# Performance work log

Hardware: AMD Instinct MI355X
Metric: run time of the kernel (lower is better)

Reference implementation:

```python
import jax, jax.numpy as jnp
import numpy as np


def setup_inputs() -> dict:
    key = jax.random.key(0)
    N, D, K = 8192, 512, 16
    x = jax.random.normal(key, (N, D), dtype=jnp.float32)
    return {"x": x, "k": K}


def reference(x, k):
    # Pairwise Euclidean distances (torch.cdist(x, x)), computed via the
    # GEMM-based expansion ||a-b||^2 = ||a||^2 + ||b||^2 - 2 a.b
    sq = jnp.sum(x * x, axis=1)                      # [N]
    d2 = sq[:, None] + sq[None, :] - 2.0 * (x @ x.T)  # [N, N]
    dists = jnp.sqrt(jnp.maximum(d2, 0.0))

    # Nearest-neighbor indices per row (skip self at column 0, since
    # self-distance is exactly 0 and therefore sorts first).
    idxs = jnp.argsort(dists, axis=1)[:, 1:k + 1]    # [N, k]

    # Gather neighbor features and average: x_avg[i] = mean(x[idxs[i]], axis=0)
    x_avg = jnp.mean(x[idxs], axis=1)                # [N, D]
    return x_avg
```

## Files before the change

### kernel.cpp

```cpp
#include <hip/hip_runtime.h>
#include <hip/hip_bf16.h>

#define Nn 8192
#define Dd 512
#define KK 16
#define CC 24
#define CSUB 5
#define JSPLIT 32
#define PENT 256

typedef int i32x4 __attribute__((ext_vector_type(4)));
typedef unsigned int uint32;

__device__ __forceinline__ uint32 med3u(uint32 a, uint32 b, uint32 c) {
  uint32 d;
  asm("v_med3_u32 %0, %1, %2, %3" : "=v"(d) : "v"(a), "v"(b), "v"(c));
  return d;
}

template <int CCn>
__device__ __forceinline__ void topk_insert(uint32* h, uint32 v) {
#pragma unroll
  for (int s = 0; s < CCn - 1; ++s) h[s] = med3u(h[s], h[s + 1], v);
  h[CCn - 1] = (h[CCn - 1] < v) ? h[CCn - 1] : v;
}

__device__ __forceinline__ uint32 cswap(uint32 v, int j, bool asc, int lane) {
  uint32 pv = (uint32)__shfl_xor((int)v, j, 64);
  uint32 mn = v < pv ? v : pv;
  uint32 mx = v < pv ? pv : v;
  const bool lower = ((lane & j) == 0);
  return (asc == lower) ? mn : mx;
}

__device__ __forceinline__ void sort64(uint32& v, int lane) {
#pragma unroll
  for (int k = 2; k <= 32; k <<= 1) {
#pragma unroll
    for (int j = k >> 1; j > 0; j >>= 1) {
      const bool asc = ((lane & k) == 0);
      v = cswap(v, j, asc, lane);
    }
  }
#pragma unroll
  for (int j = 32; j > 0; j >>= 1) v = cswap(v, j, true, lane);
}

__device__ __forceinline__ void sort128(uint32& v0, uint32& v1, int lane) {
#pragma unroll
  for (int k = 2; k <= 32; k <<= 1) {
#pragma unroll
    for (int j = k >> 1; j > 0; j >>= 1) {
      const bool asc = ((lane & k) == 0);
      v0 = cswap(v0, j, asc, lane);
      v1 = cswap(v1, j, asc, lane);
    }
  }
#pragma unroll
  for (int j = 32; j > 0; j >>= 1) {
    v0 = cswap(v0, j, true, lane);
    v1 = cswap(v1, j, false, lane);
  }
  {
    uint32 mn = v0 < v1 ? v0 : v1;
    uint32 mx = v0 < v1 ? v1 : v0;
    v0 = mn;
    v1 = mx;
  }
#pragma unroll
  for (int j = 32; j > 0; j >>= 1) {
    v0 = cswap(v0, j, true, lane);
    v1 = cswap(v1, j, true, lane);
  }
}

__global__ void knn_prep(const float* __restrict__ x, uint4* __restrict__ xq,
                         float2* __restrict__ sqs) {
  __shared__ float redS[2][16][17];
  const int rb = blockIdx.x;
  const int t = threadIdx.x;
  const int ccg = t & 15;
  const int r16 = t >> 4;
  const int row = rb * 16 + r16;
  float v[32];
  float s = 0.f, amax = 0.f;
#pragma unroll
  for (int h = 0; h < 2; ++h) {
    const int cc = h * 16 + ccg;
#pragma unroll
    for (int q = 0; q < 4; ++q) {
      float4 a = *(const float4*)&x[(size_t)row * Dd + cc * 16 + q * 4];
      v[h * 16 + q * 4 + 0] = a.x;
      v[h * 16 + q * 4 + 1] = a.y;
      v[h * 16 + q * 4 + 2] = a.z;
      v[h * 16 + q * 4 + 3] = a.w;
      s = fmaf(a.x, a.x, s); s = fmaf(a.y, a.y, s);
      s = fmaf(a.z, a.z, s); s = fmaf(a.w, a.w, s);
      amax = fmaxf(amax, fmaxf(fmaxf(fabsf(a.x), fabsf(a.y)),
                               fmaxf(fabsf(a.z), fabsf(a.w))));
    }
  }
  redS[0][r16][ccg] = s;
  redS[1][r16][ccg] = amax;
  __syncthreads();
  float tot = 0.f, mx = 0.f;
#pragma unroll
  for (int i = 0; i < 16; ++i) {
    tot += redS[0][r16][i];
    mx = fmaxf(mx, redS[1][r16][i]);
  }
  const float inv = (mx > 0.f) ? (127.f / mx) : 0.f;
  if (ccg == 0) sqs[row] = make_float2(tot, mx * (1.f / 127.f));
#pragma unroll
  for (int h = 0; h < 2; ++h) {
    const int cc = h * 16 + ccg;
    uint32 wds[4];
#pragma unroll
    for (int q = 0; q < 4; ++q) {
      uint32 b = 0;
#pragma unroll
      for (int e = 0; e < 4; ++e) {
        int qi = __float2int_rn(v[h * 16 + q * 4 + e] * inv);
        b |= ((uint32)(qi & 0xFF)) << (8 * e);
      }
      wds[q] = b;
    }
    xq[((size_t)cc * 512 + rb) * 16 + r16] =
        make_uint4(wds[0], wds[1], wds[2], wds[3]);
  }
}

__global__ __launch_bounds__(256, 2) void knn_cand(
    const uint4* __restrict__ xqv, const float2* __restrict__ sqs,
    uint32* __restrict__ partials) {
  __shared__ uint32 entS[128][41];
  __shared__ uint32 hS[128][16];

  const int bid = blockIdx.x;
  const int xcd = bid & 7;
  const int jc = xcd * 4 + ((bid >> 3) & 3);
  const int ib = bid >> 5;
  const int t = threadIdx.x;
  const int w = t >> 6;
  const int l = t & 63;
  const int wrow = w >> 1, wcol = w & 1;
  const int l16 = l & 15, lq = l >> 4;

  const i32x4* xf = (const i32x4*)xqv;
  const int abase = ib * 8 + wrow * 4;
  const int bbase = jc * 16 + wcol * 8;
  const int jbase = jc * 256;

  const i32x4* pA0 = xf + ((size_t)lq * 512 + abase) * 16 + l16;
  const i32x4* pB0 = xf + ((size_t)lq * 512 + bbase) * 16 + l16;

#define LDSET(fa, fb, s)                                              \
  do {                                                                \
    const i32x4* pa = pA0 + (size_t)(s)*32768;                        \
    const i32x4* pb = pB0 + (size_t)(s)*32768;                        \
    _Pragma("unroll") for (int q = 0; q < 4; ++q) fa[q] = pa[q * 16]; \
    _Pragma("unroll") for (int q = 0; q < 8; ++q) fb[q] = pb[q * 16]; \
  } while (0)

  uint32 heap[4][CSUB];
#pragma unroll
  for (int fi = 0; fi < 4; ++fi)
#pragma unroll
    for (int s = 0; s < CSUB; ++s) heap[fi][s] = 0xFFFFFFFFu;

  i32x4 acc[4][8];
#pragma unroll
  for (int a = 0; a < 4; ++a)
#pragma unroll
    for (int b = 0; b < 8; ++b) acc[a][b] = (i32x4){0, 0, 0, 0};

  i32x4 fa0[4], fb0[8], fa1[4], fb1[8];
  LDSET(fa0, fb0, 0);

#pragma unroll 1
  for (int s = 0; s < 8; s += 2) {
    LDSET(fa1, fb1, s + 1);
    __builtin_amdgcn_s_setprio(1);
#pragma unroll
    for (int fi = 0; fi < 4; ++fi)
#pragma unroll
      for (int fj = 0; fj < 8; ++fj)
        acc[fi][fj] = __builtin_amdgcn_mfma_i32_16x16x64_i8(
            fb0[fj], fa0[fi], acc[fi][fj], 0, 0, 0);
    __builtin_amdgcn_s_setprio(0);
    if (s + 2 < 8) LDSET(fa0, fb0, s + 2);
    __builtin_amdgcn_s_setprio(1);
#pragma unroll
    for (int fi = 0; fi < 4; ++fi)
#pragma unroll
      for (int fj = 0; fj < 8; ++fj)
        acc[fi][fj] = __builtin_amdgcn_mfma_i32_16x16x64_i8(
            fb1[fj], fa1[fi], acc[fi][fj], 0, 0, 0);
    __builtin_amdgcn_s_setprio(0);
  }
#undef LDSET

  float mi[4];
#pragma unroll
  for (int fi = 0; fi < 4; ++fi)
    mi[fi] = -2.f * sqs[ib * 128 + wrow * 64 + fi * 16 + l16].y;
  const uint32 jg_base = (uint32)(jbase + wcol * 128 + lq * 4);
#pragma unroll
  for (int fj = 0; fj < 8; ++fj) {
    const float2* sp = &sqs[jbase + wcol * 128 + fj * 16 + lq * 4];
    float4 p0 = *(const float4*)sp;
    float4 p1 = *(const float4*)(sp + 2);
    const float sv[4] = {p0.x, p0.z, p1.x, p1.z};
    const float ss[4] = {p0.y, p0.w, p1.y, p1.w};
#pragma unroll
    for (int r = 0; r < 4; ++r) {
      const uint32 jg = jg_base + (uint32)(fj * 16 + r);
#pragma unroll
      for (int fi = 0; fi < 4; ++fi) {
        float key =
            fmaxf(fmaf(mi[fi] * ss[r], (float)acc[fi][fj][r], sv[r]), 0.f);
        uint32 packed = (__builtin_bit_cast(uint32, key) & 0xFFFFE000u) | jg;
        topk_insert<CSUB>(heap[fi], packed);
      }
    }
  }

#pragma unroll
  for (int fi = 0; fi < 4; ++fi)
#pragma unroll
    for (int s = 0; s < CSUB; ++s)
      entS[wrow * 64 + fi * 16 + l16][(wcol * 4 + lq) * CSUB + s] =
          heap[fi][s];
  __syncthreads();

  const int row_s = t >> 1, half = t & 1;
  uint32 mh[8];
#pragma unroll
  for (int s = 0; s < 8; ++s) mh[s] = 0xFFFFFFFFu;
#pragma unroll
  for (int e = 0; e < 20; ++e)
    topk_insert<8>(mh, entS[row_s][half * 20 + e]);
#pragma unroll
  for (int s = 0; s < 8; ++s) hS[row_s][half * 8 + s] = mh[s];
  __syncthreads();
  if (!half) {
#pragma unroll
    for (int e = 0; e < 8; ++e) topk_insert<8>(mh, hS[row_s][8 + e]);
    const int irow = ib * 128 + row_s;
#pragma unroll
    for (int s = 0; s < 8; ++s)
      partials[(size_t)irow * PENT + jc * 8 + s] = mh[s];
  }
}

__global__ __launch_bounds__(256) void knn_rescore(
    const float* __restrict__ x, const uint32* __restrict__ partials,
    float* __restrict__ out) {
  __shared__ uint32 topS[96];
  __shared__ int candS[CC];
  __shared__ double d2S[CC];
  __shared__ int selS[KK];
  const int row = blockIdx.x;
  const int t = threadIdx.x, w = t >> 6, l = t & 63;

  {
    uint32 v = partials[(size_t)row * PENT + w * 64 + l];
    if ((v & 0x1FFFu) == (uint32)row) v = 0xFFFFFFFFu;
    sort64(v, l);
    if (l < 24) topS[w * 24 + l] = v;
  }
  __syncthreads();
  if (w == 0) {
    uint32 u0 = topS[l];
    uint32 u1 = (l < 32) ? topS[64 + l] : 0xFFFFFFFFu;
    sort128(u0, u1, l);
    if (l < CC) candS[l] = (int)(u0 & 0x1FFFu);
  }
  __syncthreads();

  const float4* x4 = (const float4*)x;
  float4 xi0 = x4[(size_t)row * 128 + l];
  float4 xi1 = x4[(size_t)row * 128 + 64 + l];
#pragma unroll
  for (int u = 0; u < 6; ++u) {
    const int c = w * 6 + u;
    const int j = candS[c];
    float4 b0 = x4[(size_t)j * 128 + l];
    float4 b1 = x4[(size_t)j * 128 + 64 + l];
    double s = 0.0;
    double d0 = (double)xi0.x - (double)b0.x;
    double d1 = (double)xi0.y - (double)b0.y;
    double d2 = (double)xi0.z - (double)b0.z;
    double d3 = (double)xi0.w - (double)b0.w;
    s = fma(d0, d0, s); s = fma(d1, d1, s); s = fma(d2, d2, s); s = fma(d3, d3, s);
    d0 = (double)xi1.x - (double)b1.x;
    d1 = (double)xi1.y - (double)b1.y;
    d2 = (double)xi1.z - (double)b1.z;
    d3 = (double)xi1.w - (double)b1.w;
    s = fma(d0, d0, s); s = fma(d1, d1, s); s = fma(d2, d2, s); s = fma(d3, d3, s);
#pragma unroll
    for (int off = 32; off > 0; off >>= 1) s += __shfl_down(s, off);
    if (l == 0) d2S[c] = s;
  }
  __syncthreads();
  if (t < CC) {
    const double mine = d2S[t];
    const int mi = candS[t];
    int rank = 0;
#pragma unroll
    for (int o = 0; o < CC; ++o) {
      double vo = d2S[o];
      int io = candS[o];
      if (vo < mine || (vo == mine && io < mi)) rank++;
    }
    if (rank < KK) selS[rank] = mi;
  }
  __syncthreads();
  const float2* x2 = (const float2*)x;
  float ax = 0.f, ay = 0.f;
#pragma unroll
  for (int n = 0; n < KK; ++n) {
    float2 vb = x2[(size_t)selS[n] * 256 + t];
    ax += vb.x;
    ay += vb.y;
  }
  ((float2*)out)[(size_t)row * 256 + t] = make_float2(ax * 0.0625f, ay * 0.0625f);
}

extern "C" void kernel_launch(void* const* d_in, const int* in_sizes, int n_in,
                              void* d_out, int out_size, void* d_ws,
                              size_t ws_size, hipStream_t stream) {
  const float* x = (const float*)d_in[0];
  float* out = (float*)d_out;
  char* ws = (char*)d_ws;
  uint4* xq = (uint4*)ws;
  float2* sqs = (float2*)(ws + (size_t)Nn * Dd);
  uint32* partials = (uint32*)(ws + (size_t)Nn * Dd + (size_t)Nn * 8);

  knn_prep<<<Nn / 16, 256, 0, stream>>>(x, xq, sqs);
  knn_cand<<<64 * JSPLIT, 256, 0, stream>>>(xq, sqs, partials);
  knn_rescore<<<Nn, 256, 0, stream>>>(x, partials, out);
}
```

Baseline: 114.8 us.

## Rescore one row per wavefront with fp32 distances and fp64 fallback on ties

The rescore kernel now assigns one row to each wavefront instead of one per block. A single 256-element bitonic sort in registers replaces the two-stage shared-memory sort, and shuffles and ballots replace the block barriers. Candidate distances are computed in fp32, and the fp64 recompute runs only when the gap between the 16th and 17th distances falls below a threshold. This removes syncs, shared memory traffic and most double-precision work, at the risk of selecting a different neighbor when fp32 ordering errs beyond the gap threshold.

```diff
diff --git a/kernel.cpp b/kernel.cpp
--- a/kernel.cpp
+++ b/kernel.cpp
@@ -8,6 +8,7 @@
 #define CSUB 5
 #define JSPLIT 32
 #define PENT 256
+#define GAPTHR 0.01f
 
 typedef int i32x4 __attribute__((ext_vector_type(4)));
 typedef unsigned int uint32;
@@ -33,20 +34,15 @@
   return (asc == lower) ? mn : mx;
 }
 
-__device__ __forceinline__ void sort64(uint32& v, int lane) {
-#pragma unroll
-  for (int k = 2; k <= 32; k <<= 1) {
-#pragma unroll
-    for (int j = k >> 1; j > 0; j >>= 1) {
-      const bool asc = ((lane & k) == 0);
-      v = cswap(v, j, asc, lane);
-    }
-  }
-#pragma unroll
-  for (int j = 32; j > 0; j >>= 1) v = cswap(v, j, true, lane);
-}
-
-__device__ __forceinline__ void sort128(uint32& v0, uint32& v1, int lane) {
+__device__ __forceinline__ void cmpx(uint32& a, uint32& b, bool asc) {
+  uint32 mn = a < b ? a : b;
+  uint32 mx = a < b ? b : a;
+  a = asc ? mn : mx;
+  b = asc ? mx : mn;
+}
+
+__device__ __forceinline__ void sort256(uint32& v0, uint32& v1, uint32& v2,
+                                        uint32& v3, int lane) {
 #pragma unroll
   for (int k = 2; k <= 32; k <<= 1) {
 #pragma unroll
@@ -54,23 +50,36 @@
       const bool asc = ((lane & k) == 0);
       v0 = cswap(v0, j, asc, lane);
       v1 = cswap(v1, j, asc, lane);
+      v2 = cswap(v2, j, asc, lane);
+      v3 = cswap(v3, j, asc, lane);
     }
   }
 #pragma unroll
   for (int j = 32; j > 0; j >>= 1) {
     v0 = cswap(v0, j, true, lane);
     v1 = cswap(v1, j, false, lane);
-  }
-  {
-    uint32 mn = v0 < v1 ? v0 : v1;
-    uint32 mx = v0 < v1 ? v1 : v0;
-    v0 = mn;
-    v1 = mx;
-  }
+    v2 = cswap(v2, j, true, lane);
+    v3 = cswap(v3, j, false, lane);
+  }
+  cmpx(v0, v1, true);
+  cmpx(v2, v3, false);
 #pragma unroll
   for (int j = 32; j > 0; j >>= 1) {
     v0 = cswap(v0, j, true, lane);
     v1 = cswap(v1, j, true, lane);
+    v2 = cswap(v2, j, false, lane);
+    v3 = cswap(v3, j, false, lane);
+  }
+  cmpx(v0, v2, true);
+  cmpx(v1, v3, true);
+  cmpx(v0, v1, true);
+  cmpx(v2, v3, true);
+#pragma unroll
+  for (int j = 32; j > 0; j >>= 1) {
+    v0 = cswap(v0, j, true, lane);
+    v1 = cswap(v1, j, true, lane);
+    v2 = cswap(v2, j, true, lane);
+    v3 = cswap(v3, j, true, lane);
   }
 }
 
@@ -256,75 +265,105 @@
 __global__ __launch_bounds__(256) void knn_rescore(
     const float* __restrict__ x, const uint32* __restrict__ partials,
     float* __restrict__ out) {
-  __shared__ uint32 topS[96];
-  __shared__ int candS[CC];
-  __shared__ double d2S[CC];
-  __shared__ int selS[KK];
-  const int row = blockIdx.x;
-  const int t = threadIdx.x, w = t >> 6, l = t & 63;
-
-  {
-    uint32 v = partials[(size_t)row * PENT + w * 64 + l];
-    if ((v & 0x1FFFu) == (uint32)row) v = 0xFFFFFFFFu;
-    sort64(v, l);
-    if (l < 24) topS[w * 24 + l] = v;
-  }
-  __syncthreads();
-  if (w == 0) {
-    uint32 u0 = topS[l];
-    uint32 u1 = (l < 32) ? topS[64 + l] : 0xFFFFFFFFu;
-    sort128(u0, u1, l);
-    if (l < CC) candS[l] = (int)(u0 & 0x1FFFu);
-  }
-  __syncthreads();
+  const int l = threadIdx.x & 63;
+  const int row = blockIdx.x * 4 + (threadIdx.x >> 6);
+
+  uint4 pv = *(const uint4*)&partials[(size_t)row * PENT + l * 4];
+  uint32 v0 = pv.x, v1 = pv.y, v2 = pv.z, v3 = pv.w;
+  if ((v0 & 0x1FFFu) == (uint32)row) v0 = 0xFFFFFFFFu;
+  if ((v1 & 0x1FFFu) == (uint32)row) v1 = 0xFFFFFFFFu;
+  if ((v2 & 0x1FFFu) == (uint32)row) v2 = 0xFFFFFFFFu;
+  if ((v3 & 0x1FFFu) == (uint32)row) v3 = 0xFFFFFFFFu;
+  sort256(v0, v1, v2, v3, l);
+  const int myj = (int)(v0 & 0x1FFFu);
 
   const float4* x4 = (const float4*)x;
   float4 xi0 = x4[(size_t)row * 128 + l];
   float4 xi1 = x4[(size_t)row * 128 + 64 + l];
-#pragma unroll
-  for (int u = 0; u < 6; ++u) {
-    const int c = w * 6 + u;
-    const int j = candS[c];
+
+  float d2v = 0.f;
+#pragma unroll
+  for (int c = 0; c < CC; ++c) {
+    const int j = __shfl(myj, c);
     float4 b0 = x4[(size_t)j * 128 + l];
     float4 b1 = x4[(size_t)j * 128 + 64 + l];
-    double s = 0.0;
-    double d0 = (double)xi0.x - (double)b0.x;
-    double d1 = (double)xi0.y - (double)b0.y;
-    double d2 = (double)xi0.z - (double)b0.z;
-    double d3 = (double)xi0.w - (double)b0.w;
-    s = fma(d0, d0, s); s = fma(d1, d1, s); s = fma(d2, d2, s); s = fma(d3, d3, s);
-    d0 = (double)xi1.x - (double)b1.x;
-    d1 = (double)xi1.y - (double)b1.y;
-    d2 = (double)xi1.z - (double)b1.z;
-    d3 = (double)xi1.w - (double)b1.w;
-    s = fma(d0, d0, s); s = fma(d1, d1, s); s = fma(d2, d2, s); s = fma(d3, d3, s);
-#pragma unroll
-    for (int off = 32; off > 0; off >>= 1) s += __shfl_down(s, off);
-    if (l == 0) d2S[c] = s;
-  }
-  __syncthreads();
-  if (t < CC) {
-    const double mine = d2S[t];
-    const int mi = candS[t];
-    int rank = 0;
+    float s = 0.f;
+    float d0 = xi0.x - b0.x, d1 = xi0.y - b0.y;
+    float d2 = xi0.z - b0.z, d3 = xi0.w - b0.w;
+    s = fmaf(d0, d0, s); s = fmaf(d1, d1, s);
+    s = fmaf(d2, d2, s); s = fmaf(d3, d3, s);
+    d0 = xi1.x - b1.x; d1 = xi1.y - b1.y;
+    d2 = xi1.z - b1.z; d3 = xi1.w - b1.w;
+    s = fmaf(d0, d0, s); s = fmaf(d1, d1, s);
+    s = fmaf(d2, d2, s); s = fmaf(d3, d3, s);
+#pragma unroll
+    for (int off = 32; off > 0; off >>= 1) s += __shfl_xor(s, off);
+    if (l == c) d2v = s;
+  }
+
+  int rank = 0;
+#pragma unroll
+  for (int o = 0; o < CC; ++o) {
+    float vo = __shfl(d2v, o);
+    int io = __shfl(myj, o);
+    if (vo < d2v || (vo == d2v && io < myj)) rank++;
+  }
+
+  unsigned long long b15 = __ballot(l < CC && rank == KK - 1);
+  unsigned long long b16 = __ballot(l < CC && rank == KK);
+  float k15 = __shfl(d2v, (int)(__ffsll(b15) - 1));
+  float k16 = __shfl(d2v, (int)(__ffsll(b16) - 1));
+  if (k16 - k15 < GAPTHR) {
+    double dd = 0.0;
+#pragma unroll
+    for (int c = 0; c < CC; ++c) {
+      const int j = __shfl(myj, c);
+      float4 b0 = x4[(size_t)j * 128 + l];
+      float4 b1 = x4[(size_t)j * 128 + 64 + l];
+      double s = 0.0;
+      double d0 = (double)xi0.x - (double)b0.x;
+      double d1 = (double)xi0.y - (double)b0.y;
+      double d2 = (double)xi0.z - (double)b0.z;
+      double d3 = (double)xi0.w - (double)b0.w;
+      s = fma(d0, d0, s); s = fma(d1, d1, s);
+      s = fma(d2, d2, s); s = fma(d3, d3, s);
+      d0 = (double)xi1.x - (double)b1.x;
+      d1 = (double)xi1.y - (double)b1.y;
+      d2 = (double)xi1.z - (double)b1.z;
+      d3 = (double)xi1.w - (double)b1.w;
+      s = fma(d0, d0, s); s = fma(d1, d1, s);
+      s = fma(d2, d2, s); s = fma(d3, d3, s);
+#pragma unroll
+      for (int off = 32; off > 0; off >>= 1) s += __shfl_xor(s, off);
+      if (l == c) dd = s;
+    }
+    rank = 0;
 #pragma unroll
     for (int o = 0; o < CC; ++o) {
-      double vo = d2S[o];
-      int io = candS[o];
-      if (vo < mine || (vo == mine && io < mi)) rank++;
-    }
-    if (rank < KK) selS[rank] = mi;
-  }
-  __syncthreads();
-  const float2* x2 = (const float2*)x;
-  float ax = 0.f, ay = 0.f;
-#pragma unroll
-  for (int n = 0; n < KK; ++n) {
-    float2 vb = x2[(size_t)selS[n] * 256 + t];
-    ax += vb.x;
-    ay += vb.y;
-  }
-  ((float2*)out)[(size_t)row * 256 + t] = make_float2(ax * 0.0625f, ay * 0.0625f);
+      double vo = __shfl(dd, o);
+      int io = __shfl(myj, o);
+      if (vo < dd || (vo == dd && io < myj)) rank++;
+    }
+  }
+
+  const unsigned long long selmask = __ballot(l < CC && rank < KK);
+  float4 a0 = make_float4(0.f, 0.f, 0.f, 0.f);
+  float4 a1 = make_float4(0.f, 0.f, 0.f, 0.f);
+#pragma unroll
+  for (int c = 0; c < CC; ++c) {
+    if ((selmask >> c) & 1ull) {
+      const int j = __shfl(myj, c);
+      float4 b0 = x4[(size_t)j * 128 + l];
+      float4 b1 = x4[(size_t)j * 128 + 64 + l];
+      a0.x += b0.x; a0.y += b0.y; a0.z += b0.z; a0.w += b0.w;
+      a1.x += b1.x; a1.y += b1.y; a1.z += b1.z; a1.w += b1.w;
+    }
+  }
+  float4* o4 = (float4*)out;
+  o4[(size_t)row * 128 + l] =
+      make_float4(a0.x * 0.0625f, a0.y * 0.0625f, a0.z * 0.0625f, a0.w * 0.0625f);
+  o4[(size_t)row * 128 + 64 + l] =
+      make_float4(a1.x * 0.0625f, a1.y * 0.0625f, a1.z * 0.0625f, a1.w * 0.0625f);
 }
 
 extern "C" void kernel_launch(void* const* d_in, const int* in_sizes, int n_in,
@@ -339,5 +378,5 @@
 
   knn_prep<<<Nn / 16, 256, 0, stream>>>(x, xq, sqs);
   knn_cand<<<64 * JSPLIT, 256, 0, stream>>>(xq, sqs, partials);
-  knn_rescore<<<Nn, 256, 0, stream>>>(x, partials, out);
-}
+  knn_rescore<<<Nn / 4, 256, 0, stream>>>(x, partials, out);
+}
```

New measurement: 103.7 us. 9.7% less time.
